# Optimization experiments

Measured on AMD Instinct MI355X. Metric: run time of the kernel, lower is better.

The kernel has to match this reference:

```python
import jax, jax.numpy as jnp
import numpy as np

B, F = 8192, 256
H1, H2, H3 = 32, 64, 32
ORDER = 2
OUT = 1


def setup_inputs() -> dict:
    key = jax.random.key(0)
    ks = jax.random.split(key, 6)
    x = jax.random.normal(ks[0], (B, F), dtype=jnp.float32)
    # stacked per-feature FeatureNet weights, fan-in scaled to keep ReLUs active
    W1 = jax.random.normal(ks[1], (F, 1, H1), dtype=jnp.float32) * 1.0
    b1 = jnp.zeros((F, H1), dtype=jnp.float32)
    W2 = jax.random.normal(ks[2], (F, H1, H2), dtype=jnp.float32) * (1.0 / np.sqrt(H1))
    b2 = jnp.zeros((F, H2), dtype=jnp.float32)
    W3 = jax.random.normal(ks[3], (F, H2, H3), dtype=jnp.float32) * (1.0 / np.sqrt(H2))
    b3 = jnp.zeros((F, H3), dtype=jnp.float32)
    Wout = jax.random.normal(ks[4], (ORDER * H3, OUT), dtype=jnp.float32) * (1.0 / np.sqrt(ORDER * H3))
    bout = jnp.zeros((OUT,), dtype=jnp.float32)
    return {"x": x, "W1": W1, "b1": b1, "W2": W2, "b2": b2,
            "W3": W3, "b3": b3, "Wout": Wout, "bout": bout}


def _feature_nets(x, W1, b1, W2, b2, W3, b3):
    # x: [B, F] -> per-feature tiny MLP 1->32->64->32, batched over F
    h = jax.nn.relu(x[:, :, None] * W1[:, 0, :][None] + b1[None])      # [B, F, 32]
    h = jax.nn.relu(jnp.einsum('bfh,fho->bfo', h, W2) + b2[None])       # [B, F, 64]
    h = jax.nn.relu(jnp.einsum('bfh,fho->bfo', h, W3) + b3[None])       # [B, F, 32]
    return h


def reference(x, W1, b1, W2, b2, W3, b3, Wout, bout):
    t = _feature_nets(x, W1, b1, W2, b2, W3, b3)  # [B, F, H3]
    # Newton's identity power-sum recurrence over interaction order
    p1 = t.sum(axis=1)                            # [B, H3]
    powers = [None, p1]                           # powers[0] unused (scalar 1 in orig)
    inters = [jnp.ones_like(p1), p1]              # interactions[0] = 1 (broadcast)
    for i in range(2, ORDER + 1):
        powers.append(jnp.power(t, i).sum(axis=1))
        cur = 0.0
        for j in range(1, i + 1):
            cur = cur + ((-1.0) ** (j + 1)) * powers[j] * inters[i - j]
        inters.append(cur / i)
    feats = jnp.concatenate(inters[1:], axis=1)   # [B, ORDER*H3]
    pred = feats @ Wout + bout                    # [B, OUT]
    return pred
```

## Files before the change

kernel.cpp:

```cpp
#include <hip/hip_runtime.h>
#include <hip/hip_bf16.h>

#define B_   8192
#define F_   256
#define NFC  16
#define NF   (F_/NFC)
#define NPH  (NF/2)
#define RPB  128
#define NSUB 2

typedef __attribute__((ext_vector_type(8))) short v8s;
typedef __attribute__((ext_vector_type(4))) float v4f;
typedef __attribute__((ext_vector_type(4))) unsigned int v4u;

static __device__ __forceinline__ unsigned short f2bf(float f) {
    __hip_bfloat16 h = __float2bfloat16(f);
    return __builtin_bit_cast(unsigned short, h);
}

static __device__ __forceinline__ unsigned cvtpk(float a, float b) {
    unsigned r;
    asm("v_cvt_pk_bf16_f32 %0, %1, %2" : "=v"(r) : "v"(a), "v"(b));
    return r;
}

static __device__ __forceinline__ void gload_lds16(const void* g, void* l) {
    __builtin_amdgcn_global_load_lds(
        (const __attribute__((address_space(1))) unsigned int*)g,
        (__attribute__((address_space(3))) unsigned int*)l,
        16, 0, 0);
}

__global__ __launch_bounds__(256)
void honam_prep(const float* __restrict__ w2g, const float* __restrict__ w3g,
                const float* __restrict__ w1g, const float* __restrict__ b1g,
                const float* __restrict__ b2g, const float* __restrict__ b3g,
                unsigned short* __restrict__ wf, float* __restrict__ pp)
{
    const int f   = blockIdx.x;
    const int tid = threadIdx.x;
    const float* w2 = w2g + (size_t)f * 2048;
    const float* w3 = w3g + (size_t)f * 2048;
    unsigned short* dst = wf + (size_t)f * 4096;
    for (int i = tid; i < 4096; i += 256) {
        const int frag = i >> 9;
        const int l    = (i >> 3) & 63;
        const int j    = i & 7;
        const int c    = l & 15;
        const int g    = l >> 4;
        float v;
        if (frag < 4) {
            v = w2[(g * 8 + j) * 64 + frag * 16 + c];
        } else {
            const int kk = (frag - 4) >> 1;
            const int n2 = (frag - 4) & 1;
            const int u  = (kk * 2 + (j >> 2)) * 16 + g * 4 + (j & 3);
            v = w3[u * 32 + n2 * 16 + c];
        }
        dst[i] = f2bf(v);
    }
    if (tid < 160) {
        float v;
        if (tid < 32)       v = w1g[f * 32 + tid];
        else if (tid < 64)  v = b1g[f * 32 + (tid - 32)];
        else if (tid < 128) v = b2g[f * 64 + (tid - 64)];
        else                v = b3g[f * 32 + (tid - 128)];
        pp[(size_t)f * 160 + tid] = v;
    }
}

__global__ __launch_bounds__(256, 2)
void honam_k1(const float* __restrict__ xg,
              const unsigned short* __restrict__ wfg, const float* __restrict__ ppg,
              float* __restrict__ p1part, float* __restrict__ p2part)
{
    __shared__ float xs[NF][RPB];
    __shared__ float ps[NF * 160];
    __shared__ short wbuf[2][2][4096] __attribute__((aligned(16)));

    const int tid  = threadIdx.x;
    const int wave = tid >> 6;
    const int lane = tid & 63;
    const int c16  = lane & 15;
    const int g4   = lane >> 4;

    const int bx = blockIdx.x;
    const int rb = bx >> 4;
    const int fc = bx & 15;
    const int r0 = rb * RPB;
    const int f0 = fc * NF;

    {
        const int row  = tid >> 1;
        const int half = tid & 1;
        const float4 va = *(const float4*)&xg[(size_t)(r0 + row) * F_ + f0 + half * 8];
        const float4 vb = *(const float4*)&xg[(size_t)(r0 + row) * F_ + f0 + half * 8 + 4];
        const int fb = half * 8;
        xs[fb + 0][row] = va.x; xs[fb + 1][row] = va.y;
        xs[fb + 2][row] = va.z; xs[fb + 3][row] = va.w;
        xs[fb + 4][row] = vb.x; xs[fb + 5][row] = vb.y;
        xs[fb + 6][row] = vb.z; xs[fb + 7][row] = vb.w;
    }
    {
        const float4* src = (const float4*)(ppg + (size_t)f0 * 160);
        float4* dst = (float4*)ps;
        dst[tid]       = src[tid];
        dst[tid + 256] = src[tid + 256];
        if (tid < 128) dst[tid + 512] = src[tid + 512];
    }

    auto stage = [&](int set, int fp, int fl) {
        const char* src = (const char*)wfg + (size_t)(f0 + fl) * 8192
                        + (2 * wave) * 1024 + lane * 16;
        gload_lds16(src,        &wbuf[set][fp][(2 * wave) * 512]);
        gload_lds16(src + 1024, &wbuf[set][fp][(2 * wave + 1) * 512]);
    };

    stage(0, 0, 0);
    stage(0, 1, 1);
    __syncthreads();

    float2 pacc1[NSUB][2][2];
    float2 pacc2[NSUB][2][2];
#pragma unroll
    for (int s = 0; s < NSUB; ++s)
#pragma unroll
        for (int n2 = 0; n2 < 2; ++n2)
#pragma unroll
            for (int jp = 0; jp < 2; ++jp) {
                pacc1[s][n2][jp] = make_float2(0.f, 0.f);
                pacc2[s][n2][jp] = make_float2(0.f, 0.f);
            }

    auto computeFeat = [&](int set, int fp, int fl) {
        const short* wb = &wbuf[set][fp][0];
        v8s wfr[8];
#pragma unroll
        for (int fr = 0; fr < 8; ++fr)
            wfr[fr] = *(const v8s*)&wb[fr * 512 + lane * 8];

        const int fb = fl * 160;
        const float4 w1a = *(const float4*)&ps[fb + g4 * 8];
        const float4 w1b = *(const float4*)&ps[fb + g4 * 8 + 4];
        const float4 b1a = *(const float4*)&ps[fb + 32 + g4 * 8];
        const float4 b1b = *(const float4*)&ps[fb + 32 + g4 * 8 + 4];
        const float w1v[8] = {w1a.x, w1a.y, w1a.z, w1a.w, w1b.x, w1b.y, w1b.z, w1b.w};
        const float b1v[8] = {b1a.x, b1a.y, b1a.z, b1a.w, b1b.x, b1b.y, b1b.z, b1b.w};
        float b3v[2];
#pragma unroll
        for (int n = 0; n < 2; ++n) b3v[n] = ps[fb + 128 + n * 16 + c16];

        float xm[NSUB];
#pragma unroll
        for (int s = 0; s < NSUB; ++s)
            xm[s] = xs[fl][s * 64 + wave * 16 + c16];

#pragma unroll
        for (int sub = 0; sub < NSUB; ++sub) {
            unsigned h1p[4];
#pragma unroll
            for (int jj = 0; jj < 4; ++jj) {
                const float e0 = fmaxf(fmaf(xm[sub], w1v[2 * jj],     b1v[2 * jj]),     0.f);
                const float e1 = fmaxf(fmaf(xm[sub], w1v[2 * jj + 1], b1v[2 * jj + 1]), 0.f);
                h1p[jj] = cvtpk(e0, e1);
            }
            const v8s bh1 = __builtin_bit_cast(v8s, (v4u){h1p[0], h1p[1], h1p[2], h1p[3]});

            __builtin_amdgcn_s_setprio(1);
            v4f acc2[4];
#pragma unroll
            for (int n = 0; n < 4; ++n) {
                const v4f b2cv = *(const v4f*)&ps[fb + 64 + n * 16 + g4 * 4];
                acc2[n] = __builtin_amdgcn_mfma_f32_16x16x32_bf16(wfr[n], bh1, b2cv, 0, 0, 0);
            }
            __builtin_amdgcn_s_setprio(0);

            unsigned q[8];
#pragma unroll
            for (int n = 0; n < 4; ++n) {
                q[2 * n]     = cvtpk(fmaxf(acc2[n][0], 0.f), fmaxf(acc2[n][1], 0.f));
                q[2 * n + 1] = cvtpk(fmaxf(acc2[n][2], 0.f), fmaxf(acc2[n][3], 0.f));
            }
            const v8s a2k0 = __builtin_bit_cast(v8s, (v4u){q[0], q[1], q[2], q[3]});
            const v8s a2k1 = __builtin_bit_cast(v8s, (v4u){q[4], q[5], q[6], q[7]});

            __builtin_amdgcn_s_setprio(1);
            v4f acc3[2];
#pragma unroll
            for (int n2 = 0; n2 < 2; ++n2) {
                acc3[n2] = __builtin_amdgcn_mfma_f32_16x16x32_bf16(
                    a2k0, wfr[4 + n2], (v4f){b3v[n2], b3v[n2], b3v[n2], b3v[n2]}, 0, 0, 0);
                acc3[n2] = __builtin_amdgcn_mfma_f32_16x16x32_bf16(
                    a2k1, wfr[6 + n2], acc3[n2], 0, 0, 0);
            }
            __builtin_amdgcn_s_setprio(0);
#pragma unroll
            for (int n2 = 0; n2 < 2; ++n2)
#pragma unroll
                for (int jp = 0; jp < 2; ++jp) {
                    float2 t;
                    t.x = fmaxf(acc3[n2][2 * jp],     0.f);
                    t.y = fmaxf(acc3[n2][2 * jp + 1], 0.f);
                    pacc1[sub][n2][jp].x += t.x;
                    pacc1[sub][n2][jp].y += t.y;
                    pacc2[sub][n2][jp].x += t.x * t.x;
                    pacc2[sub][n2][jp].y += t.y * t.y;
                }
        }
    };

#pragma unroll 2
    for (int ph = 0; ph < NPH; ++ph) {
        const int set = ph & 1;
        if (ph + 1 < NPH) {
            stage(set ^ 1, 0, 2 * ph + 2);
            stage(set ^ 1, 1, 2 * ph + 3);
        }
        computeFeat(set, 0, 2 * ph);
        computeFeat(set, 1, 2 * ph + 1);
        __syncthreads();
    }

    float* p1c = p1part + (size_t)fc * (B_ * 32);
    float* p2c = p2part + (size_t)fc * (B_ * 32);
#pragma unroll
    for (int sub = 0; sub < NSUB; ++sub)
#pragma unroll
        for (int n2 = 0; n2 < 2; ++n2)
#pragma unroll
            for (int jp = 0; jp < 2; ++jp) {
                const int row = r0 + sub * 64 + wave * 16 + g4 * 4 + 2 * jp;
                const int col = n2 * 16 + c16;
                p1c[row * 32 + col]       = pacc1[sub][n2][jp].x;
                p1c[(row + 1) * 32 + col] = pacc1[sub][n2][jp].y;
                p2c[row * 32 + col]       = pacc2[sub][n2][jp].x;
                p2c[(row + 1) * 32 + col] = pacc2[sub][n2][jp].y;
            }
}

__global__ __launch_bounds__(256)
void honam_k2(const float* __restrict__ p1part, const float* __restrict__ p2part,
              const float* __restrict__ woutg, const float* __restrict__ boutg,
              float* __restrict__ outg)
{
    const int tid = threadIdx.x;
    const int o   = tid & 31;
    const int r   = blockIdx.x * 8 + (tid >> 5);
    const size_t idx = (size_t)r * 32 + o;

    float s1 = 0.f, s2 = 0.f;
#pragma unroll
    for (int fc = 0; fc < NFC; ++fc) {
        s1 += p1part[(size_t)fc * (B_ * 32) + idx];
        s2 += p2part[(size_t)fc * (B_ * 32) + idx];
    }
    const float wa = woutg[o];
    const float wb = woutg[32 + o];
    float val = s1 * wa + 0.5f * (s1 * s1 - s2) * wb;
#pragma unroll
    for (int off = 16; off > 0; off >>= 1)
        val += __shfl_down(val, off, 32);
    if (o == 0) outg[r] = val + boutg[0];
}

extern "C" void kernel_launch(void* const* d_in, const int* in_sizes, int n_in,
                              void* d_out, int out_size, void* d_ws, size_t ws_size,
                              hipStream_t stream)
{
    const float* xg    = (const float*)d_in[0];
    const float* w1g   = (const float*)d_in[1];
    const float* b1g   = (const float*)d_in[2];
    const float* w2g   = (const float*)d_in[3];
    const float* b2g   = (const float*)d_in[4];
    const float* w3g   = (const float*)d_in[5];
    const float* b3g   = (const float*)d_in[6];
    const float* woutg = (const float*)d_in[7];
    const float* boutg = (const float*)d_in[8];
    float* outg = (float*)d_out;

    float* p1part = (float*)d_ws;
    float* p2part = p1part + (size_t)NFC * B_ * 32;
    unsigned short* wf = (unsigned short*)(p2part + (size_t)NFC * B_ * 32);
    float* pp = (float*)(wf + (size_t)F_ * 4096);

    honam_prep<<<dim3(F_), dim3(256), 0, stream>>>(w2g, w3g, w1g, b1g, b2g, b3g, wf, pp);

    honam_k1<<<dim3((B_ / RPB) * NFC), dim3(256), 0, stream>>>(
        xg, wf, pp, p1part, p2part);

    honam_k2<<<dim3(B_ / 8), dim3(256), 0, stream>>>(p1part, p2part, woutg, boutg, outg);
}
```

Measured before the change: 51.83 us.

## Halve feature chunks per block, use packed f32 accumulation, hoist bias loads

Changes the feature split from 16 chunks to 8, so each block handles 32 features and the grid shrinks by half. This cuts the partial-sum output written per row and the reduction work after it, at the cost of fewer blocks and longer per-block loops. The p1/p2 accumulation switches to packed v_pk_add_f32 and v_pk_fma_f32, and the b2 bias loads are hoisted out of the sub-tile loop. The unroll pragma on the phase loop is also removed.

```diff
diff --git a/kernel.cpp b/kernel.cpp
--- a/kernel.cpp
+++ b/kernel.cpp
@@ -3,7 +3,7 @@
 
 #define B_   8192
 #define F_   256
-#define NFC  16
+#define NFC  8
 #define NF   (F_/NFC)
 #define NPH  (NF/2)
 #define RPB  128
@@ -11,6 +11,7 @@
 
 typedef __attribute__((ext_vector_type(8))) short v8s;
 typedef __attribute__((ext_vector_type(4))) float v4f;
+typedef __attribute__((ext_vector_type(2))) float v2f;
 typedef __attribute__((ext_vector_type(4))) unsigned int v4u;
 
 static __device__ __forceinline__ unsigned short f2bf(float f) {
@@ -22,6 +23,12 @@
     unsigned r;
     asm("v_cvt_pk_bf16_f32 %0, %1, %2" : "=v"(r) : "v"(a), "v"(b));
     return r;
+}
+static __device__ __forceinline__ v2f pk_add(v2f a, v2f b) {
+    v2f d; asm("v_pk_add_f32 %0, %1, %2" : "=v"(d) : "v"(a), "v"(b)); return d;
+}
+static __device__ __forceinline__ v2f pk_fma(v2f a, v2f b, v2f c) {
+    v2f d; asm("v_pk_fma_f32 %0, %1, %2, %3" : "=v"(d) : "v"(a), "v"(b), "v"(c)); return d;
 }
 
 static __device__ __forceinline__ void gload_lds16(const void* g, void* l) {
@@ -85,28 +92,32 @@
     const int g4   = lane >> 4;
 
     const int bx = blockIdx.x;
-    const int rb = bx >> 4;
-    const int fc = bx & 15;
+    const int rb = bx >> 3;
+    const int fc = bx & 7;
     const int r0 = rb * RPB;
     const int f0 = fc * NF;
 
     {
-        const int row  = tid >> 1;
-        const int half = tid & 1;
-        const float4 va = *(const float4*)&xg[(size_t)(r0 + row) * F_ + f0 + half * 8];
-        const float4 vb = *(const float4*)&xg[(size_t)(r0 + row) * F_ + f0 + half * 8 + 4];
-        const int fb = half * 8;
-        xs[fb + 0][row] = va.x; xs[fb + 1][row] = va.y;
-        xs[fb + 2][row] = va.z; xs[fb + 3][row] = va.w;
-        xs[fb + 4][row] = vb.x; xs[fb + 5][row] = vb.y;
-        xs[fb + 6][row] = vb.z; xs[fb + 7][row] = vb.w;
+        const int rr = tid >> 2;
+        const int q  = tid & 3;
+#pragma unroll
+        for (int p = 0; p < 2; ++p) {
+            const int row = p * 64 + rr;
+            const float4 va = *(const float4*)&xg[(size_t)(r0 + row) * F_ + f0 + q * 8];
+            const float4 vb = *(const float4*)&xg[(size_t)(r0 + row) * F_ + f0 + q * 8 + 4];
+            const int fb = q * 8;
+            xs[fb + 0][row] = va.x; xs[fb + 1][row] = va.y;
+            xs[fb + 2][row] = va.z; xs[fb + 3][row] = va.w;
+            xs[fb + 4][row] = vb.x; xs[fb + 5][row] = vb.y;
+            xs[fb + 6][row] = vb.z; xs[fb + 7][row] = vb.w;
+        }
     }
     {
         const float4* src = (const float4*)(ppg + (size_t)f0 * 160);
         float4* dst = (float4*)ps;
-        dst[tid]       = src[tid];
-        dst[tid + 256] = src[tid + 256];
-        if (tid < 128) dst[tid + 512] = src[tid + 512];
+#pragma unroll
+        for (int p = 0; p < 5; ++p)
+            dst[tid + p * 256] = src[tid + p * 256];
     }
 
     auto stage = [&](int set, int fp, int fl) {
@@ -120,16 +131,16 @@
     stage(0, 1, 1);
     __syncthreads();
 
-    float2 pacc1[NSUB][2][2];
-    float2 pacc2[NSUB][2][2];
+    v2f pacc1[NSUB][2][2];
+    v2f pacc2[NSUB][2][2];
 #pragma unroll
     for (int s = 0; s < NSUB; ++s)
 #pragma unroll
         for (int n2 = 0; n2 < 2; ++n2)
 #pragma unroll
             for (int jp = 0; jp < 2; ++jp) {
-                pacc1[s][n2][jp] = make_float2(0.f, 0.f);
-                pacc2[s][n2][jp] = make_float2(0.f, 0.f);
+                pacc1[s][n2][jp] = (v2f){0.f, 0.f};
+                pacc2[s][n2][jp] = (v2f){0.f, 0.f};
             }
 
     auto computeFeat = [&](int set, int fp, int fl) {
@@ -146,6 +157,10 @@
         const float4 b1b = *(const float4*)&ps[fb + 32 + g4 * 8 + 4];
         const float w1v[8] = {w1a.x, w1a.y, w1a.z, w1a.w, w1b.x, w1b.y, w1b.z, w1b.w};
         const float b1v[8] = {b1a.x, b1a.y, b1a.z, b1a.w, b1b.x, b1b.y, b1b.z, b1b.w};
+        v4f b2cv[4];
+#pragma unroll
+        for (int n = 0; n < 4; ++n)
+            b2cv[n] = *(const v4f*)&ps[fb + 64 + n * 16 + g4 * 4];
         float b3v[2];
 #pragma unroll
         for (int n = 0; n < 2; ++n) b3v[n] = ps[fb + 128 + n * 16 + c16];
@@ -169,10 +184,8 @@
             __builtin_amdgcn_s_setprio(1);
             v4f acc2[4];
 #pragma unroll
-            for (int n = 0; n < 4; ++n) {
-                const v4f b2cv = *(const v4f*)&ps[fb + 64 + n * 16 + g4 * 4];
-                acc2[n] = __builtin_amdgcn_mfma_f32_16x16x32_bf16(wfr[n], bh1, b2cv, 0, 0, 0);
-            }
+            for (int n = 0; n < 4; ++n)
+                acc2[n] = __builtin_amdgcn_mfma_f32_16x16x32_bf16(wfr[n], bh1, b2cv[n], 0, 0, 0);
             __builtin_amdgcn_s_setprio(0);
 
             unsigned q[8];
@@ -198,18 +211,15 @@
             for (int n2 = 0; n2 < 2; ++n2)
 #pragma unroll
                 for (int jp = 0; jp < 2; ++jp) {
-                    float2 t;
+                    v2f t;
                     t.x = fmaxf(acc3[n2][2 * jp],     0.f);
                     t.y = fmaxf(acc3[n2][2 * jp + 1], 0.f);
-                    pacc1[sub][n2][jp].x += t.x;
-                    pacc1[sub][n2][jp].y += t.y;
-                    pacc2[sub][n2][jp].x += t.x * t.x;
-                    pacc2[sub][n2][jp].y += t.y * t.y;
+                    pacc1[sub][n2][jp] = pk_add(pacc1[sub][n2][jp], t);
+                    pacc2[sub][n2][jp] = pk_fma(t, t, pacc2[sub][n2][jp]);
                 }
         }
     };
 
-#pragma unroll 2
     for (int ph = 0; ph < NPH; ++ph) {
         const int set = ph & 1;
         if (ph + 1 < NPH) {
```

Result: slower. 57.17 us (+10.3%).
